# Kernel optimization log

Measured on AMD Instinct MI355X. Metric: run time of the kernel, lower is better.

Reference implementation:

```python
import jax, jax.numpy as jnp
import numpy as np

B, N, D, FF = 4096, 8, 256, 2048
EPS = 1e-5


def _layernorm(x, gamma, beta):
    mu = jnp.mean(x, axis=-1, keepdims=True)
    var = jnp.mean((x - mu) ** 2, axis=-1, keepdims=True)
    return (x - mu) * jax.lax.rsqrt(var + EPS) * gamma + beta


def _tt_product(x, w):
    # x: [b, d_in, n], w: [d_in, d_out, n]
    # h[:, :, k] = sum_i x[:, :, i] @ w[:, :, (k - i) % n]  (circular contraction)
    n = x.shape[-1]
    k = jnp.arange(n)
    idx = (k[:, None] - k[None, :]) % n          # [k, i]
    wg = w[:, :, idx]                            # [d_in, d_out, k, i]
    return jnp.einsum('bdi,doki->bok', x, wg)    # [b, d_out, n]


def setup_inputs() -> dict:
    key = jax.random.key(0)
    ks = jax.random.split(key, 12)
    xav = lambda k, shp, fi, fo: jax.random.uniform(k, shp, jnp.float32, -1.0, 1.0) * np.sqrt(6.0 / (fi + fo))
    return {
        'ent_seq': jax.random.normal(ks[0], (B, N, D), jnp.float32),
        'w_in': xav(ks[1], (D, D, N), D, D),
        'w_out': xav(ks[2], (D, D, N), D, D),
        'W1': xav(ks[3], (FF, D), D, FF),
        'bias1': jnp.zeros((FF,), jnp.float32),
        'W2': xav(ks[4], (D, FF), FF, D),
        'bias2': jnp.zeros((D,), jnp.float32),
        'gamma1': jnp.ones((D,), jnp.float32),
        'beta1': jnp.zeros((D,), jnp.float32),
        'gamma2': jnp.ones((D,), jnp.float32),
        'beta2': jnp.zeros((D,), jnp.float32),
    }


def reference(ent_seq, w_in, w_out, W1, bias1, W2, bias2, gamma1, beta1, gamma2, beta2):
    # self-attention-like block (dropout = identity in eval mode)
    xn = _layernorm(ent_seq, gamma1, beta1)          # [B, N, D]
    xp = jnp.transpose(xn, (0, 2, 1))                # [B, D, N]
    half = xp.shape[0] // 2
    h = jnp.concatenate([_tt_product(xp[:half], w_in),
                         _tt_product(xp[half:], w_out)], axis=0)
    x = ent_seq + jnp.transpose(h, (0, 2, 1))        # residual
    # FFN block
    yn = _layernorm(x, gamma2, beta2)
    ff = jax.nn.relu(yn @ W1.T + bias1) @ W2.T + bias2
    return x + ff
```

## Files before the change

kernel.cpp:

```cpp
#include <hip/hip_runtime.h>
#include <hip/hip_bf16.h>

typedef unsigned short ushort_t;
typedef __attribute__((ext_vector_type(8))) short bf16x8;
typedef __attribute__((ext_vector_type(4))) float f32x4;

#define B_SZ 4096
#define N_SZ 8
#define D_SZ 256
#define FF_SZ 2048
#define M_SZ (B_SZ * N_SZ)
#define WELEM (D_SZ * D_SZ * N_SZ)

__device__ inline float b2f(ushort_t u) {
    union { unsigned int i; float f; } t; t.i = ((unsigned int)u) << 16; return t.f;
}
__device__ inline ushort_t f2b(float f) {
    union { unsigned int i; float f; } t; t.f = f;
    unsigned int i = t.i;
    unsigned int r = (i + 0x7fffu + ((i >> 16) & 1u)) >> 16;
    return (ushort_t)r;
}

__device__ inline void gl2lds16(const ushort_t* g, ushort_t* l) {
    __builtin_amdgcn_global_load_lds((const __attribute__((address_space(1))) void*)g,
                                     (__attribute__((address_space(3))) void*)l, 16, 0, 0);
}

__global__ __launch_bounds__(256) void convert_weights(const float* __restrict__ w_in,
                                                       const float* __restrict__ w_out,
                                                       const float* __restrict__ W1,
                                                       const float* __restrict__ W2,
                                                       ushort_t* __restrict__ bt_in,
                                                       ushort_t* __restrict__ bt_out,
                                                       ushort_t* __restrict__ W1b,
                                                       ushort_t* __restrict__ W2b) {
    __shared__ float tile[64][65];
    const int bid = blockIdx.x;
    const int t = threadIdx.x;
    if (bid < 256) {
        const float* w = (bid < 128) ? w_in : w_out;
        ushort_t* bt = (bid < 128) ? bt_in : bt_out;
        const int id = bid & 127;
        const int d10 = (id >> 5) * 64;
        const int j0  = (id & 31) * 64;
#pragma unroll
        for (int it = 0; it < 16; ++it) {
            const int d1l = it * 4 + (t >> 6);
            const int jl = t & 63;
            tile[d1l][jl] = w[(size_t)(d10 + d1l) * 2048 + j0 + jl];
        }
        __syncthreads();
#pragma unroll
        for (int it = 0; it < 16; ++it) {
            const int jl = it * 4 + (t >> 6);
            const int d1l = t & 63;
            const int j = j0 + jl;
            bt[(size_t)(j >> 3) * 2048 + (j & 7) * 256 + d10 + d1l] = f2b(tile[d1l][jl]);
        }
    } else {
        const int id = bid - 256;
        const float* w = (id < 256) ? W1 : W2;
        ushort_t* o = (id < 256) ? W1b : W2b;
        const size_t base = (size_t)(id & 255) * 2048 + t * 8;
        const float4 a = *(const float4*)&w[base];
        const float4 b = *(const float4*)&w[base + 4];
        *(ushort4*)&o[base]     = make_ushort4(f2b(a.x), f2b(a.y), f2b(a.z), f2b(a.w));
        *(ushort4*)&o[base + 4] = make_ushort4(f2b(b.x), f2b(b.y), f2b(b.z), f2b(b.w));
    }
}

__global__ __launch_bounds__(256) void ln_fast(const float* __restrict__ xin,
                                               const float* __restrict__ gam,
                                               const float* __restrict__ bet,
                                               ushort_t* __restrict__ out) {
    const int wave = threadIdx.x >> 6;
    const int lane = threadIdx.x & 63;
    const size_t row = (size_t)blockIdx.x * 4 + wave;
    const float4 v = *(const float4*)&xin[row * 256 + lane * 4];
    float s = v.x + v.y + v.z + v.w;
    float q = v.x * v.x + v.y * v.y + v.z * v.z + v.w * v.w;
#pragma unroll
    for (int off = 1; off < 64; off <<= 1) {
        s += __shfl_xor(s, off, 64);
        q += __shfl_xor(q, off, 64);
    }
    const float mu = s * (1.0f / 256.0f);
    const float var = q * (1.0f / 256.0f) - mu * mu;
    const float rs = rsqrtf(var + 1e-5f);
    const float4 g = *(const float4*)&gam[lane * 4];
    const float4 b = *(const float4*)&bet[lane * 4];
    ushort4 o;
    o.x = f2b((v.x - mu) * rs * g.x + b.x);
    o.y = f2b((v.y - mu) * rs * g.y + b.y);
    o.z = f2b((v.z - mu) * rs * g.z + b.z);
    o.w = f2b((v.w - mu) * rs * g.w + b.w);
    *(ushort4*)&out[row * 256 + lane * 4] = o;
}

__global__ __launch_bounds__(512) void tt_ln2(const ushort_t* __restrict__ A,
                                              const ushort_t* __restrict__ Bt0,
                                              const ushort_t* __restrict__ Bt1,
                                              const float* __restrict__ g2,
                                              const float* __restrict__ be2,
                                              const float* __restrict__ entf,
                                              ushort_t* __restrict__ yn,
                                              ushort_t* __restrict__ xb) {
    __shared__ __attribute__((aligned(16))) ushort_t As[128 * 64];
    __shared__ __attribute__((aligned(16))) ushort_t Bs[256 * 64];
    __shared__ float red_s[128 * 4];
    __shared__ float red_q[128 * 4];

    const int t = threadIdx.x;
    const int m0 = blockIdx.x * 128;
    const int lane = t & 63;
    const int wave = t >> 6;
    const int wr = wave & 1, wc = wave >> 1;
    const int l16 = lane & 15, quad = lane >> 4;
    const int tr = t >> 3;
    const int csw = (((t & 7) ^ (tr & 7)) << 3);

    const ushort_t* Bt = (m0 >= M_SZ / 2) ? Bt1 : Bt0;

    f32x4 acc[4][4];
#pragma unroll
    for (int i = 0; i < 4; i++)
#pragma unroll
        for (int j = 0; j < 4; j++) acc[i][j] = (f32x4)(0.0f);

    for (int kt = 0; kt < 32; ++kt) {
        const int kg = kt * 64;
        __syncthreads();
#pragma unroll
        for (int p = 0; p < 2; ++p) {
            const int mrow = m0 + p * 64 + tr;
            const int kcol = kg + csw;
            const int s = kcol >> 8;
            const ushort_t* gA = A + (size_t)((mrow & ~7) + (((mrow & 7) - s) & 7)) * 256 + (kcol & 255);
            gl2lds16(gA, As + p * 4096 + t * 8);
        }
#pragma unroll
        for (int p = 0; p < 4; ++p) {
            gl2lds16(Bt + (size_t)(p * 64 + tr) * 2048 + kg + csw, Bs + p * 4096 + t * 8);
        }
        __syncthreads();

#pragma unroll
        for (int kk = 0; kk < 2; ++kk) {
            const int ac = ((((kk << 2) | quad) ^ (l16 & 7)) << 3);
            bf16x8 af[4], bfv[4];
#pragma unroll
            for (int i = 0; i < 4; i++) af[i]  = *(const bf16x8*)&As[(wr * 64 + i * 16 + l16) * 64 + ac];
#pragma unroll
            for (int j = 0; j < 4; j++) bfv[j] = *(const bf16x8*)&Bs[(wc * 64 + j * 16 + l16) * 64 + ac];
#pragma unroll
            for (int i = 0; i < 4; i++)
#pragma unroll
                for (int j = 0; j < 4; j++)
                    acc[i][j] = __builtin_amdgcn_mfma_f32_16x16x32_bf16(af[i], bfv[j], acc[i][j], 0, 0, 0);
        }
    }

    int c[4];
#pragma unroll
    for (int j = 0; j < 4; j++) c[j] = wc * 64 + j * 16 + l16;
#pragma unroll
    for (int i = 0; i < 4; i++) {
#pragma unroll
        for (int r = 0; r < 4; r++) {
            const int rl = wr * 64 + i * 16 + quad * 4 + r;
            const size_t grow = (size_t)(m0 + rl) * 256;
            float s = 0.0f, q = 0.0f;
#pragma unroll
            for (int j = 0; j < 4; j++) {
                float v = acc[i][j][r] + entf[grow + c[j]];
                acc[i][j][r] = v;
                s += v;
                q += v * v;
            }
#pragma unroll
            for (int off = 1; off < 16; off <<= 1) {
                s += __shfl_xor(s, off, 64);
                q += __shfl_xor(q, off, 64);
            }
            if (l16 == 0) { red_s[rl * 4 + wc] = s; red_q[rl * 4 + wc] = q; }
        }
    }
    __syncthreads();
#pragma unroll
    for (int i = 0; i < 4; i++) {
#pragma unroll
        for (int r = 0; r < 4; r++) {
            const int rl = wr * 64 + i * 16 + quad * 4 + r;
            const size_t grow = (size_t)(m0 + rl) * 256;
            const float4 ss = *(const float4*)&red_s[rl * 4];
            const float4 qq = *(const float4*)&red_q[rl * 4];
            const float S = ss.x + ss.y + ss.z + ss.w;
            const float Q = qq.x + qq.y + qq.z + qq.w;
            const float mu = S * (1.0f / 256.0f);
            const float var = Q * (1.0f / 256.0f) - mu * mu;
            const float rs = rsqrtf(var + 1e-5f);
#pragma unroll
            for (int j = 0; j < 4; j++) {
                const float v = acc[i][j][r];
                yn[grow + c[j]] = f2b((v - mu) * rs * g2[c[j]] + be2[c[j]]);
                xb[grow + c[j]] = f2b(v);
            }
        }
    }
}

#define HSTRIDE 272
__global__ __launch_bounds__(512) void ff_fused(const ushort_t* __restrict__ yn,
                                                const ushort_t* __restrict__ W1b,
                                                const ushort_t* __restrict__ W2b,
                                                const float* __restrict__ bias1,
                                                const float* __restrict__ bias2,
                                                const ushort_t* __restrict__ xb,
                                                float* __restrict__ out) {
    __shared__ __attribute__((aligned(16))) ushort_t As[128 * 64];
    __shared__ __attribute__((aligned(16))) ushort_t Bs[256 * 64];
    __shared__ __attribute__((aligned(16))) ushort_t Hc[128 * HSTRIDE];

    const int t = threadIdx.x;
    const int m0 = blockIdx.x * 128;
    const int lane = t & 63;
    const int wave = t >> 6;
    const int wr = wave & 1, wc = wave >> 1;
    const int l16 = lane & 15, quad = lane >> 4;
    const int tr = t >> 3;
    const int csw = (((t & 7) ^ (tr & 7)) << 3);

    f32x4 acc2[4][4];
#pragma unroll
    for (int i = 0; i < 4; i++)
#pragma unroll
        for (int j = 0; j < 4; j++) acc2[i][j] = (f32x4)(0.0f);

    int c4[4];
#pragma unroll
    for (int j = 0; j < 4; j++) c4[j] = wc * 64 + j * 16 + l16;

    for (int c = 0; c < 8; ++c) {
        f32x4 acc1[4][4];
#pragma unroll
        for (int i = 0; i < 4; i++)
#pragma unroll
            for (int j = 0; j < 4; j++) acc1[i][j] = (f32x4)(0.0f);

        for (int kb = 0; kb < 4; ++kb) {
            const int kg = kb * 64;
            __syncthreads();
#pragma unroll
            for (int p = 0; p < 2; ++p) {
                gl2lds16(yn + (size_t)(m0 + p * 64 + tr) * 256 + kg + csw, As + p * 4096 + t * 8);
            }
#pragma unroll
            for (int p = 0; p < 4; ++p) {
                gl2lds16(W1b + (size_t)(c * 256 + p * 64 + tr) * 256 + kg + csw, Bs + p * 4096 + t * 8);
            }
            __syncthreads();
#pragma unroll
            for (int kk = 0; kk < 2; ++kk) {
                const int ac = ((((kk << 2) | quad) ^ (l16 & 7)) << 3);
                bf16x8 af[4], bfv[4];
#pragma unroll
                for (int i = 0; i < 4; i++) af[i]  = *(const bf16x8*)&As[(wr * 64 + i * 16 + l16) * 64 + ac];
#pragma unroll
                for (int j = 0; j < 4; j++) bfv[j] = *(const bf16x8*)&Bs[(wc * 64 + j * 16 + l16) * 64 + ac];
#pragma unroll
                for (int i = 0; i < 4; i++)
#pragma unroll
                    for (int j = 0; j < 4; j++)
                        acc1[i][j] = __builtin_amdgcn_mfma_f32_16x16x32_bf16(af[i], bfv[j], acc1[i][j], 0, 0, 0);
            }
        }

        __syncthreads();

#pragma unroll
        for (int j = 0; j < 4; j++) {
            const float bb = bias1[c * 256 + c4[j]];
#pragma unroll
            for (int i = 0; i < 4; i++) {
                const int rbase = wr * 64 + i * 16 + quad * 4;
#pragma unroll
                for (int r = 0; r < 4; r++) {
                    float v = acc1[i][j][r] + bb;
                    v = v > 0.0f ? v : 0.0f;
                    Hc[(rbase + r) * HSTRIDE + c4[j]] = f2b(v);
                }
            }
        }

        for (int kb = 0; kb < 4; ++kb) {
            __syncthreads();
#pragma unroll
            for (int p = 0; p < 4; ++p) {
                gl2lds16(W2b + (size_t)(p * 64 + tr) * 2048 + c * 256 + kb * 64 + csw, Bs + p * 4096 + t * 8);
            }
            __syncthreads();
#pragma unroll
            for (int kk = 0; kk < 2; ++kk) {
                const int ank = kb * 64 + (((kk << 2) | quad) << 3);
                const int ac = ((((kk << 2) | quad) ^ (l16 & 7)) << 3);
                bf16x8 af[4], bfv[4];
#pragma unroll
                for (int i = 0; i < 4; i++) af[i]  = *(const bf16x8*)&Hc[(wr * 64 + i * 16 + l16) * HSTRIDE + ank];
#pragma unroll
                for (int j = 0; j < 4; j++) bfv[j] = *(const bf16x8*)&Bs[(wc * 64 + j * 16 + l16) * 64 + ac];
#pragma unroll
                for (int i = 0; i < 4; i++)
#pragma unroll
                    for (int j = 0; j < 4; j++)
                        acc2[i][j] = __builtin_amdgcn_mfma_f32_16x16x32_bf16(af[i], bfv[j], acc2[i][j], 0, 0, 0);
            }
        }
    }

#pragma unroll
    for (int j = 0; j < 4; j++) {
        const float b2 = bias2[c4[j]];
#pragma unroll
        for (int i = 0; i < 4; i++) {
            const int rbase = m0 + wr * 64 + i * 16 + quad * 4;
#pragma unroll
            for (int r = 0; r < 4; r++) {
                const size_t o = (size_t)(rbase + r) * 256 + c4[j];
                out[o] = acc2[i][j][r] + b2 + b2f(xb[o]);
            }
        }
    }
}

extern "C" void kernel_launch(void* const* d_in, const int* in_sizes, int n_in,
                              void* d_out, int out_size, void* d_ws, size_t ws_size,
                              hipStream_t stream) {
    const float* ent   = (const float*)d_in[0];
    const float* w_in  = (const float*)d_in[1];
    const float* w_out = (const float*)d_in[2];
    const float* W1    = (const float*)d_in[3];
    const float* bias1 = (const float*)d_in[4];
    const float* W2    = (const float*)d_in[5];
    const float* bias2 = (const float*)d_in[6];
    const float* g1    = (const float*)d_in[7];
    const float* be1   = (const float*)d_in[8];
    const float* g2    = (const float*)d_in[9];
    const float* be2   = (const float*)d_in[10];
    float* out = (float*)d_out;

    char* ws = (char*)d_ws;
    ushort_t* xn     = (ushort_t*)ws;
    ushort_t* yn     = (ushort_t*)(ws + 16777216);
    ushort_t* xb     = (ushort_t*)(ws + 2 * 16777216);
    ushort_t* bt_in  = (ushort_t*)(ws + 3 * 16777216);
    ushort_t* bt_out = bt_in + WELEM;
    ushort_t* W1b    = bt_out + WELEM;
    ushort_t* W2b    = W1b + WELEM;

    convert_weights<<<dim3(768), dim3(256), 0, stream>>>(w_in, w_out, W1, W2,
                                                         bt_in, bt_out, W1b, W2b);
    ln_fast<<<dim3(M_SZ / 4), dim3(256), 0, stream>>>(ent, g1, be1, xn);
    tt_ln2<<<dim3(M_SZ / 128), dim3(512), 0, stream>>>(xn, bt_in, bt_out, g2, be2, ent, yn, xb);
    ff_fused<<<dim3(M_SZ / 128), dim3(512), 0, stream>>>(yn, W1b, W2b, bias1, bias2, xb, out);
}
```

Baseline: 259.8 us.

## Double-buffer LDS tiles in both GEMM kernels and swizzle the hidden-activation buffer

Both the TT-product/LN2 kernel and the fused FFN kernel now keep two LDS buffers for the A and B tiles. Each k-step prefetches the next tile, including across the GEMM1/GEMM2 boundary and into the next FF chunk, so only one barrier per step is needed and global loads can overlap MFMA work. The padded Hc buffer (stride 272) is replaced by an unpadded 256-wide buffer with an XOR swizzle to avoid LDS bank conflicts while saving space. The larger LDS footprint (about 160KB in ff_fused, about 100KB in tt_ln2) cuts how many blocks fit per CU, which may offset the overlap gain.

New measurement: 254.1 us. 1.02x faster.

```diff
diff --git a/kernel.cpp b/kernel.cpp
--- a/kernel.cpp
+++ b/kernel.cpp
@@ -106,8 +106,8 @@
                                               const float* __restrict__ entf,
                                               ushort_t* __restrict__ yn,
                                               ushort_t* __restrict__ xb) {
-    __shared__ __attribute__((aligned(16))) ushort_t As[128 * 64];
-    __shared__ __attribute__((aligned(16))) ushort_t Bs[256 * 64];
+    __shared__ __attribute__((aligned(16))) ushort_t As[2][128 * 64];
+    __shared__ __attribute__((aligned(16))) ushort_t Bs[2][256 * 64];
     __shared__ float red_s[128 * 4];
     __shared__ float red_q[128 * 4];
 
@@ -128,31 +128,39 @@
 #pragma unroll
         for (int j = 0; j < 4; j++) acc[i][j] = (f32x4)(0.0f);
 
-    for (int kt = 0; kt < 32; ++kt) {
+    auto stage = [&](int kt) {
+        ushort_t* a = As[kt & 1];
+        ushort_t* b = Bs[kt & 1];
         const int kg = kt * 64;
-        __syncthreads();
 #pragma unroll
         for (int p = 0; p < 2; ++p) {
             const int mrow = m0 + p * 64 + tr;
             const int kcol = kg + csw;
             const int s = kcol >> 8;
             const ushort_t* gA = A + (size_t)((mrow & ~7) + (((mrow & 7) - s) & 7)) * 256 + (kcol & 255);
-            gl2lds16(gA, As + p * 4096 + t * 8);
+            gl2lds16(gA, a + p * 4096 + t * 8);
         }
 #pragma unroll
         for (int p = 0; p < 4; ++p) {
-            gl2lds16(Bt + (size_t)(p * 64 + tr) * 2048 + kg + csw, Bs + p * 4096 + t * 8);
-        }
+            gl2lds16(Bt + (size_t)(p * 64 + tr) * 2048 + kg + csw, b + p * 4096 + t * 8);
+        }
+    };
+
+    stage(0);
+#pragma unroll 2
+    for (int kt = 0; kt < 32; ++kt) {
         __syncthreads();
-
+        if (kt < 31) stage(kt + 1);
+        const ushort_t* a = As[kt & 1];
+        const ushort_t* b = Bs[kt & 1];
 #pragma unroll
         for (int kk = 0; kk < 2; ++kk) {
             const int ac = ((((kk << 2) | quad) ^ (l16 & 7)) << 3);
             bf16x8 af[4], bfv[4];
 #pragma unroll
-            for (int i = 0; i < 4; i++) af[i]  = *(const bf16x8*)&As[(wr * 64 + i * 16 + l16) * 64 + ac];
-#pragma unroll
-            for (int j = 0; j < 4; j++) bfv[j] = *(const bf16x8*)&Bs[(wc * 64 + j * 16 + l16) * 64 + ac];
+            for (int i = 0; i < 4; i++) af[i]  = *(const bf16x8*)&a[(wr * 64 + i * 16 + l16) * 64 + ac];
+#pragma unroll
+            for (int j = 0; j < 4; j++) bfv[j] = *(const bf16x8*)&b[(wc * 64 + j * 16 + l16) * 64 + ac];
 #pragma unroll
             for (int i = 0; i < 4; i++)
 #pragma unroll
@@ -210,7 +218,6 @@
     }
 }
 
-#define HSTRIDE 272
 __global__ __launch_bounds__(512) void ff_fused(const ushort_t* __restrict__ yn,
                                                 const ushort_t* __restrict__ W1b,
                                                 const ushort_t* __restrict__ W2b,
@@ -218,9 +225,9 @@
                                                 const float* __restrict__ bias2,
                                                 const ushort_t* __restrict__ xb,
                                                 float* __restrict__ out) {
-    __shared__ __attribute__((aligned(16))) ushort_t As[128 * 64];
-    __shared__ __attribute__((aligned(16))) ushort_t Bs[256 * 64];
-    __shared__ __attribute__((aligned(16))) ushort_t Hc[128 * HSTRIDE];
+    __shared__ __attribute__((aligned(16))) ushort_t As[2][128 * 64];
+    __shared__ __attribute__((aligned(16))) ushort_t Bs[2][256 * 64];
+    __shared__ __attribute__((aligned(16))) ushort_t Hc[128 * 256];
 
     const int t = threadIdx.x;
     const int m0 = blockIdx.x * 128;
@@ -241,6 +248,27 @@
 #pragma unroll
     for (int j = 0; j < 4; j++) c4[j] = wc * 64 + j * 16 + l16;
 
+    auto stage_g1 = [&](int cc, int kb) {
+        ushort_t* a = As[kb & 1];
+        ushort_t* b = Bs[kb & 1];
+        const int kg = kb * 64;
+#pragma unroll
+        for (int p = 0; p < 2; ++p)
+            gl2lds16(yn + (size_t)(m0 + p * 64 + tr) * 256 + kg + csw, a + p * 4096 + t * 8);
+#pragma unroll
+        for (int p = 0; p < 4; ++p)
+            gl2lds16(W1b + (size_t)(cc * 256 + p * 64 + tr) * 256 + kg + csw, b + p * 4096 + t * 8);
+    };
+    auto stage_g2 = [&](int cc, int kb) {
+        ushort_t* b = Bs[kb & 1];
+#pragma unroll
+        for (int p = 0; p < 4; ++p)
+            gl2lds16(W2b + (size_t)(p * 64 + tr) * 2048 + cc * 256 + kb * 64 + csw, b + p * 4096 + t * 8);
+    };
+
+    stage_g1(0, 0);
+
+#pragma unroll 1
     for (int c = 0; c < 8; ++c) {
         f32x4 acc1[4][4];
 #pragma unroll
@@ -248,26 +276,21 @@
 #pragma unroll
             for (int j = 0; j < 4; j++) acc1[i][j] = (f32x4)(0.0f);
 
+#pragma unroll
         for (int kb = 0; kb < 4; ++kb) {
-            const int kg = kb * 64;
             __syncthreads();
-#pragma unroll
-            for (int p = 0; p < 2; ++p) {
-                gl2lds16(yn + (size_t)(m0 + p * 64 + tr) * 256 + kg + csw, As + p * 4096 + t * 8);
-            }
-#pragma unroll
-            for (int p = 0; p < 4; ++p) {
-                gl2lds16(W1b + (size_t)(c * 256 + p * 64 + tr) * 256 + kg + csw, Bs + p * 4096 + t * 8);
-            }
-            __syncthreads();
+            if (kb < 3) stage_g1(c, kb + 1);
+            else        stage_g2(c, 0);
+            const ushort_t* a = As[kb & 1];
+            const ushort_t* b = Bs[kb & 1];
 #pragma unroll
             for (int kk = 0; kk < 2; ++kk) {
                 const int ac = ((((kk << 2) | quad) ^ (l16 & 7)) << 3);
                 bf16x8 af[4], bfv[4];
 #pragma unroll
-                for (int i = 0; i < 4; i++) af[i]  = *(const bf16x8*)&As[(wr * 64 + i * 16 + l16) * 64 + ac];
-#pragma unroll
-                for (int j = 0; j < 4; j++) bfv[j] = *(const bf16x8*)&Bs[(wc * 64 + j * 16 + l16) * 64 + ac];
+                for (int i = 0; i < 4; i++) af[i]  = *(const bf16x8*)&a[(wr * 64 + i * 16 + l16) * 64 + ac];
+#pragma unroll
+                for (int j = 0; j < 4; j++) bfv[j] = *(const bf16x8*)&b[(wc * 64 + j * 16 + l16) * 64 + ac];
 #pragma unroll
                 for (int i = 0; i < 4; i++)
 #pragma unroll
@@ -276,8 +299,6 @@
             }
         }
 
-        __syncthreads();
-
 #pragma unroll
         for (int j = 0; j < 4; j++) {
             const float bb = bias1[c * 256 + c4[j]];
@@ -286,29 +307,30 @@
                 const int rbase = wr * 64 + i * 16 + quad * 4;
 #pragma unroll
                 for (int r = 0; r < 4; r++) {
+                    const int row = rbase + r;
                     float v = acc1[i][j][r] + bb;
                     v = v > 0.0f ? v : 0.0f;
-                    Hc[(rbase + r) * HSTRIDE + c4[j]] = f2b(v);
+                    Hc[row * 256 + (c4[j] ^ ((row & 7) << 3))] = f2b(v);
                 }
             }
         }
 
+#pragma unroll
         for (int kb = 0; kb < 4; ++kb) {
             __syncthreads();
-#pragma unroll
-            for (int p = 0; p < 4; ++p) {
-                gl2lds16(W2b + (size_t)(p * 64 + tr) * 2048 + c * 256 + kb * 64 + csw, Bs + p * 4096 + t * 8);
-            }
-            __syncthreads();
+            if (kb < 3)      stage_g2(c, kb + 1);
+            else if (c < 7)  stage_g1(c + 1, 0);
+            const ushort_t* b = Bs[kb & 1];
 #pragma unroll
             for (int kk = 0; kk < 2; ++kk) {
                 const int ank = kb * 64 + (((kk << 2) | quad) << 3);
-                const int ac = ((((kk << 2) | quad) ^ (l16 & 7)) << 3);
+                const int ah  = ank ^ ((l16 & 7) << 3);
+                const int ac  = ((((kk << 2) | quad) ^ (l16 & 7)) << 3);
                 bf16x8 af[4], bfv[4];
 #pragma unroll
-                for (int i = 0; i < 4; i++) af[i]  = *(const bf16x8*)&Hc[(wr * 64 + i * 16 + l16) * HSTRIDE + ank];
-#pragma unroll
-                for (int j = 0; j < 4; j++) bfv[j] = *(const bf16x8*)&Bs[(wc * 64 + j * 16 + l16) * 64 + ac];
+                for (int i = 0; i < 4; i++) af[i]  = *(const bf16x8*)&Hc[(wr * 64 + i * 16 + l16) * 256 + ah];
+#pragma unroll
+                for (int j = 0; j < 4; j++) bfv[j] = *(const bf16x8*)&b[(wc * 64 + j * 16 + l16) * 64 + ac];
 #pragma unroll
                 for (int i = 0; i < 4; i++)
 #pragma unroll
```

## Shrink GEMM tiles to 64 rows with 4 waves and swizzle H buffer

Applied to the files above, without the earlier changes.

Both fused GEMM kernels move from 128-row tiles with 8 waves to 64-row tiles with 4 waves, launch twice as many blocks, and request two blocks per CU. The hidden-activation buffer switches from a padded stride to an XOR-swizzled 256-wide layout, which shrinks LDS use, and a redundant barrier before writing it is removed. tt_ln2 also interleaves block indices so blocks using the two weight sets alternate. The aim is higher occupancy and better latency hiding, at the cost of each weight tile being reused by half as many rows, so more weight traffic from global memory.

Measured after the change: 244.2 us. -6.0%, faster.

```diff
diff --git a/kernel.cpp b/kernel.cpp
--- a/kernel.cpp
+++ b/kernel.cpp
@@ -98,24 +98,24 @@
     *(ushort4*)&out[row * 256 + lane * 4] = o;
 }
 
-__global__ __launch_bounds__(512) void tt_ln2(const ushort_t* __restrict__ A,
-                                              const ushort_t* __restrict__ Bt0,
-                                              const ushort_t* __restrict__ Bt1,
-                                              const float* __restrict__ g2,
-                                              const float* __restrict__ be2,
-                                              const float* __restrict__ entf,
-                                              ushort_t* __restrict__ yn,
-                                              ushort_t* __restrict__ xb) {
-    __shared__ __attribute__((aligned(16))) ushort_t As[128 * 64];
+__global__ __launch_bounds__(256, 2) void tt_ln2(const ushort_t* __restrict__ A,
+                                                 const ushort_t* __restrict__ Bt0,
+                                                 const ushort_t* __restrict__ Bt1,
+                                                 const float* __restrict__ g2,
+                                                 const float* __restrict__ be2,
+                                                 const float* __restrict__ entf,
+                                                 ushort_t* __restrict__ yn,
+                                                 ushort_t* __restrict__ xb) {
+    __shared__ __attribute__((aligned(16))) ushort_t As[64 * 64];
     __shared__ __attribute__((aligned(16))) ushort_t Bs[256 * 64];
-    __shared__ float red_s[128 * 4];
-    __shared__ float red_q[128 * 4];
+    __shared__ float red_s[64 * 4];
+    __shared__ float red_q[64 * 4];
 
     const int t = threadIdx.x;
-    const int m0 = blockIdx.x * 128;
+    const int lb = ((blockIdx.x & 1) << 8) | (blockIdx.x >> 1);
+    const int m0 = lb * 64;
     const int lane = t & 63;
-    const int wave = t >> 6;
-    const int wr = wave & 1, wc = wave >> 1;
+    const int wc = t >> 6;
     const int l16 = lane & 15, quad = lane >> 4;
     const int tr = t >> 3;
     const int csw = (((t & 7) ^ (tr & 7)) << 3);
@@ -128,20 +128,21 @@
 #pragma unroll
         for (int j = 0; j < 4; j++) acc[i][j] = (f32x4)(0.0f);
 
+#pragma unroll 1
     for (int kt = 0; kt < 32; ++kt) {
         const int kg = kt * 64;
         __syncthreads();
 #pragma unroll
         for (int p = 0; p < 2; ++p) {
-            const int mrow = m0 + p * 64 + tr;
+            const int mrow = m0 + p * 32 + tr;
             const int kcol = kg + csw;
             const int s = kcol >> 8;
             const ushort_t* gA = A + (size_t)((mrow & ~7) + (((mrow & 7) - s) & 7)) * 256 + (kcol & 255);
-            gl2lds16(gA, As + p * 4096 + t * 8);
-        }
-#pragma unroll
-        for (int p = 0; p < 4; ++p) {
-            gl2lds16(Bt + (size_t)(p * 64 + tr) * 2048 + kg + csw, Bs + p * 4096 + t * 8);
+            gl2lds16(gA, As + p * 2048 + t * 8);
+        }
+#pragma unroll
+        for (int p = 0; p < 8; ++p) {
+            gl2lds16(Bt + (size_t)(p * 32 + tr) * 2048 + kg + csw, Bs + p * 2048 + t * 8);
         }
         __syncthreads();
 
@@ -150,7 +151,7 @@
             const int ac = ((((kk << 2) | quad) ^ (l16 & 7)) << 3);
             bf16x8 af[4], bfv[4];
 #pragma unroll
-            for (int i = 0; i < 4; i++) af[i]  = *(const bf16x8*)&As[(wr * 64 + i * 16 + l16) * 64 + ac];
+            for (int i = 0; i < 4; i++) af[i]  = *(const bf16x8*)&As[(i * 16 + l16) * 64 + ac];
 #pragma unroll
             for (int j = 0; j < 4; j++) bfv[j] = *(const bf16x8*)&Bs[(wc * 64 + j * 16 + l16) * 64 + ac];
 #pragma unroll
@@ -168,7 +169,7 @@
     for (int i = 0; i < 4; i++) {
 #pragma unroll
         for (int r = 0; r < 4; r++) {
-            const int rl = wr * 64 + i * 16 + quad * 4 + r;
+            const int rl = i * 16 + quad * 4 + r;
             const size_t grow = (size_t)(m0 + rl) * 256;
             float s = 0.0f, q = 0.0f;
 #pragma unroll
@@ -191,7 +192,7 @@
     for (int i = 0; i < 4; i++) {
 #pragma unroll
         for (int r = 0; r < 4; r++) {
-            const int rl = wr * 64 + i * 16 + quad * 4 + r;
+            const int rl = i * 16 + quad * 4 + r;
             const size_t grow = (size_t)(m0 + rl) * 256;
             const float4 ss = *(const float4*)&red_s[rl * 4];
             const float4 qq = *(const float4*)&red_q[rl * 4];
@@ -210,23 +211,21 @@
     }
 }
 
-#define HSTRIDE 272
-__global__ __launch_bounds__(512) void ff_fused(const ushort_t* __restrict__ yn,
-                                                const ushort_t* __restrict__ W1b,
-                                                const ushort_t* __restrict__ W2b,
-                                                const float* __restrict__ bias1,
-                                                const float* __restrict__ bias2,
-                                                const ushort_t* __restrict__ xb,
-                                                float* __restrict__ out) {
-    __shared__ __attribute__((aligned(16))) ushort_t As[128 * 64];
+__global__ __launch_bounds__(256, 2) void ff_fused(const ushort_t* __restrict__ yn,
+                                                   const ushort_t* __restrict__ W1b,
+                                                   const ushort_t* __restrict__ W2b,
+                                                   const float* __restrict__ bias1,
+                                                   const float* __restrict__ bias2,
+                                                   const ushort_t* __restrict__ xb,
+                                                   float* __restrict__ out) {
+    __shared__ __attribute__((aligned(16))) ushort_t As[64 * 64];
     __shared__ __attribute__((aligned(16))) ushort_t Bs[256 * 64];
-    __shared__ __attribute__((aligned(16))) ushort_t Hc[128 * HSTRIDE];
+    __shared__ __attribute__((aligned(16))) ushort_t Hc[64 * 256];
 
     const int t = threadIdx.x;
-    const int m0 = blockIdx.x * 128;
+    const int m0 = blockIdx.x * 64;
     const int lane = t & 63;
-    const int wave = t >> 6;
-    const int wr = wave & 1, wc = wave >> 1;
+    const int wc = t >> 6;
     const int l16 = lane & 15, quad = lane >> 4;
     const int tr = t >> 3;
     const int csw = (((t & 7) ^ (tr & 7)) << 3);
@@ -241,6 +240,7 @@
 #pragma unroll
     for (int j = 0; j < 4; j++) c4[j] = wc * 64 + j * 16 + l16;
 
+#pragma unroll 1
     for (int c = 0; c < 8; ++c) {
         f32x4 acc1[4][4];
 #pragma unroll
@@ -248,24 +248,23 @@
 #pragma unroll
             for (int j = 0; j < 4; j++) acc1[i][j] = (f32x4)(0.0f);
 
+#pragma unroll 1
         for (int kb = 0; kb < 4; ++kb) {
             const int kg = kb * 64;
             __syncthreads();
 #pragma unroll
-            for (int p = 0; p < 2; ++p) {
-                gl2lds16(yn + (size_t)(m0 + p * 64 + tr) * 256 + kg + csw, As + p * 4096 + t * 8);
-            }
-#pragma unroll
-            for (int p = 0; p < 4; ++p) {
-                gl2lds16(W1b + (size_t)(c * 256 + p * 64 + tr) * 256 + kg + csw, Bs + p * 4096 + t * 8);
-            }
+            for (int p = 0; p < 2; ++p)
+                gl2lds16(yn + (size_t)(m0 + p * 32 + tr) * 256 + kg + csw, As + p * 2048 + t * 8);
+#pragma unroll
+            for (int p = 0; p < 8; ++p)
+                gl2lds16(W1b + (size_t)(c * 256 + p * 32 + tr) * 256 + kg + csw, Bs + p * 2048 + t * 8);
             __syncthreads();
 #pragma unroll
             for (int kk = 0; kk < 2; ++kk) {
                 const int ac = ((((kk << 2) | quad) ^ (l16 & 7)) << 3);
                 bf16x8 af[4], bfv[4];
 #pragma unroll
-                for (int i = 0; i < 4; i++) af[i]  = *(const bf16x8*)&As[(wr * 64 + i * 16 + l16) * 64 + ac];
+                for (int i = 0; i < 4; i++) af[i]  = *(const bf16x8*)&As[(i * 16 + l16) * 64 + ac];
 #pragma unroll
                 for (int j = 0; j < 4; j++) bfv[j] = *(const bf16x8*)&Bs[(wc * 64 + j * 16 + l16) * 64 + ac];
 #pragma unroll
@@ -276,37 +275,37 @@
             }
         }
 
-        __syncthreads();
-
 #pragma unroll
         for (int j = 0; j < 4; j++) {
             const float bb = bias1[c * 256 + c4[j]];
 #pragma unroll
             for (int i = 0; i < 4; i++) {
-                const int rbase = wr * 64 + i * 16 + quad * 4;
+                const int rbase = i * 16 + quad * 4;
 #pragma unroll
                 for (int r = 0; r < 4; r++) {
+                    const int row = rbase + r;
                     float v = acc1[i][j][r] + bb;
                     v = v > 0.0f ? v : 0.0f;
-                    Hc[(rbase + r) * HSTRIDE + c4[j]] = f2b(v);
+                    Hc[row * 256 + (c4[j] ^ ((row & 7) << 3))] = f2b(v);
                 }
             }
         }
 
+#pragma unroll 1
         for (int kb = 0; kb < 4; ++kb) {
             __syncthreads();
 #pragma unroll
-            for (int p = 0; p < 4; ++p) {
-                gl2lds16(W2b + (size_t)(p * 64 + tr) * 2048 + c * 256 + kb * 64 + csw, Bs + p * 4096 + t * 8);
-            }
+            for (int p = 0; p < 8; ++p)
+                gl2lds16(W2b + (size_t)(p * 32 + tr) * 2048 + c * 256 + kb * 64 + csw, Bs + p * 2048 + t * 8);
             __syncthreads();
 #pragma unroll
             for (int kk = 0; kk < 2; ++kk) {
                 const int ank = kb * 64 + (((kk << 2) | quad) << 3);
-                const int ac = ((((kk << 2) | quad) ^ (l16 & 7)) << 3);
+                const int ah  = ank ^ ((l16 & 7) << 3);
+                const int ac  = ((((kk << 2) | quad) ^ (l16 & 7)) << 3);
                 bf16x8 af[4], bfv[4];
 #pragma unroll
-                for (int i = 0; i < 4; i++) af[i]  = *(const bf16x8*)&Hc[(wr * 64 + i * 16 + l16) * HSTRIDE + ank];
+                for (int i = 0; i < 4; i++) af[i]  = *(const bf16x8*)&Hc[(i * 16 + l16) * 256 + ah];
 #pragma unroll
                 for (int j = 0; j < 4; j++) bfv[j] = *(const bf16x8*)&Bs[(wc * 64 + j * 16 + l16) * 64 + ac];
 #pragma unroll
@@ -323,7 +322,7 @@
         const float b2 = bias2[c4[j]];
 #pragma unroll
         for (int i = 0; i < 4; i++) {
-            const int rbase = m0 + wr * 64 + i * 16 + quad * 4;
+            const int rbase = m0 + i * 16 + quad * 4;
 #pragma unroll
             for (int r = 0; r < 4; r++) {
                 const size_t o = (size_t)(rbase + r) * 256 + c4[j];
@@ -361,6 +360,6 @@
     convert_weights<<<dim3(768), dim3(256), 0, stream>>>(w_in, w_out, W1, W2,
                                                          bt_in, bt_out, W1b, W2b);
     ln_fast<<<dim3(M_SZ / 4), dim3(256), 0, stream>>>(ent, g1, be1, xn);
-    tt_ln2<<<dim3(M_SZ / 128), dim3(512), 0, stream>>>(xn, bt_in, bt_out, g2, be2, ent, yn, xb);
-    ff_fused<<<dim3(M_SZ / 128), dim3(512), 0, stream>>>(yn, W1b, W2b, bias1, bias2, xb, out);
-}
+    tt_ln2<<<dim3(M_SZ / 64), dim3(256), 0, stream>>>(xn, bt_in, bt_out, g2, be2, ent, yn, xb);
+    ff_fused<<<dim3(M_SZ / 64), dim3(256), 0, stream>>>(yn, W1b, W2b, bias1, bias2, xb, out);
+}
```
